# Performance work log

Measured on AMD Instinct MI355X. Metric: run time of the kernel, lower is better.

The kernel has to match this reference:

```python
import jax, jax.numpy as jnp
import numpy as np
from jax import lax

B, C_IN, N, C_OUT, K = 8, 64, 4096, 64, 20
EPS = 1e-5
NEG_SLOPE = 0.2


def setup_inputs() -> dict:
    key = jax.random.key(0)
    k1, k2, k3, k4, k5, k6 = jax.random.split(key, 6)
    x = jax.random.normal(k1, (B, C_IN, N), dtype=jnp.float32)
    # Conv2d(2*C_in, C_out, kernel_size=1, bias=False) -> weight (C_out, 2*C_in)
    W = jax.random.normal(k2, (C_OUT, 2 * C_IN), dtype=jnp.float32) * (1.0 / np.sqrt(2 * C_IN))
    gamma = jax.random.normal(k3, (C_OUT,), dtype=jnp.float32) * 0.1 + 1.0
    beta = jax.random.normal(k4, (C_OUT,), dtype=jnp.float32) * 0.1
    running_mean = jax.random.normal(k5, (C_OUT,), dtype=jnp.float32) * 0.1
    running_var = jax.random.uniform(k6, (C_OUT,), dtype=jnp.float32, minval=0.5, maxval=1.5)
    return {"x": x, "W": W, "gamma": gamma, "beta": beta,
            "running_mean": running_mean, "running_var": running_var}


def reference(x, W, gamma, beta, running_mean, running_var):
    # x: (B, C, N)
    # ---- KNN graph: pairwise squared distances, top-k nearest (includes self) ----
    xx = jnp.sum(x * x, axis=1)                       # (B, N)
    inner = jnp.einsum('bcn,bcm->bnm', x, x)          # (B, N, N)
    d2 = xx[:, :, None] - 2.0 * inner + xx[:, None, :]  # (B, N, N)
    _, idx = lax.top_k(-d2, K)                        # (B, N, K) int32 indices

    # ---- gather neighbor features ----
    xt = jnp.transpose(x, (0, 2, 1))                  # (B, N, C)
    neighbors = jax.vmap(lambda feats, i: feats[i])(xt, idx)  # (B, N, K, C)
    central = xt[:, :, None, :]                       # (B, N, 1, C) broadcast over K

    # ---- edge features: [x_i, x_j - x_i] -> (B, N, K, 2C) ----
    edge = jnp.concatenate(
        [jnp.broadcast_to(central, (B, N, K, C_IN)), neighbors - central], axis=-1)

    # ---- 1x1 conv (pointwise matmul) + BatchNorm (eval mode) + LeakyReLU ----
    h = jnp.einsum('bnkc,oc->bnko', edge, W)          # (B, N, K, C_out)
    inv_std = lax.rsqrt(running_var + EPS)
    h = (h - running_mean) * (inv_std * gamma) + beta
    h = jnp.where(h >= 0, h, NEG_SLOPE * h)           # LeakyReLU(0.2)

    # ---- max over k neighbors, return (B, C_out, N) ----
    out = jnp.max(h, axis=2)                          # (B, N, C_out)
    return jnp.transpose(out, (0, 2, 1))
```

## Files before the change

### kernel.cpp

```cpp
#include <hip/hip_runtime.h>

#define NB 8
#define NC 64
#define NN 4096
#define NO 64
#define KK 20
#define EPSV 1e-5f
#define SLOPE 0.2f

typedef __attribute__((ext_vector_type(8))) short short8x;
typedef __attribute__((ext_vector_type(4))) float float4x;


__device__ __forceinline__ unsigned short bfh(float f) {
  unsigned u = __float_as_uint(f);
  unsigned r = u + 0x7FFFu + ((u >> 16) & 1u);
  return (unsigned short)(r >> 16);
}

__device__ __forceinline__ unsigned flipf(float f) {
  unsigned u = __float_as_uint(f);
  return u ^ ((unsigned)((int)u >> 31) | 0x80000000u);
}

__device__ __forceinline__ unsigned unflipu(unsigned v) {
  return v ^ (0x80000000u | (unsigned)((int)(~v) >> 31));
}

__device__ __forceinline__ void gld_lds16(const unsigned short* g, unsigned short* l) {
  __builtin_amdgcn_global_load_lds(
      (const __attribute__((address_space(1))) unsigned int*)g,
      (__attribute__((address_space(3))) unsigned int*)l, 16, 0, 0);
}

__global__ void k0_wprep(const float* __restrict__ W,
                         float* __restrict__ wa, float* __restrict__ wb) {
  int t = threadIdx.x;
  for (int i = t; i < NC * NO; i += 256) {
    int o = i & 63, c = i >> 6;
    float w1 = W[o * 128 + c];
    float w2 = W[o * 128 + 64 + c];
    wa[i] = w1 - w2;
    wb[i] = w2;
  }
}

__global__ __launch_bounds__(256) void k1_feat(const float* __restrict__ x,
    const float* __restrict__ waT, const float* __restrict__ wbT,
    float* __restrict__ y1, float* __restrict__ y2, float* __restrict__ xxg,
    unsigned short* __restrict__ xThi, unsigned short* __restrict__ xTmid,
    unsigned short* __restrict__ xTlo) {
  __shared__ __align__(16) float xs[NC * 68];
  __shared__ __align__(16) float wa[NC * NO];
  __shared__ __align__(16) float wb[NC * NO];
  int t = threadIdx.x;
  int b = blockIdx.x >> 6;
  int gr0 = (blockIdx.x & 63) << 6;
  const float* xb = x + (size_t)b * NC * NN;
  #pragma unroll
  for (int k = 0; k < 4; ++k) {
    int i4 = t + k * 256;
    int c = i4 >> 4, col4 = (i4 & 15) << 2;
    *(float4*)&xs[c * 68 + col4] = *(const float4*)&xb[(size_t)c * NN + gr0 + col4];
    *(float4*)&wa[c * 64 + col4] = *(const float4*)&waT[c * 64 + col4];
    *(float4*)&wb[c * 64 + col4] = *(const float4*)&wbT[c * 64 + col4];
  }
  __syncthreads();
  if (t < 64) {
    float s = 0.f;
    #pragma unroll
    for (int c = 0; c < NC; ++c) { float v = xs[c * 68 + t]; s = fmaf(v, v, s); }
    xxg[b * NN + gr0 + t] = s;
  }
  int o = t & 63, w = t >> 6;
  for (int j = 0; j < 16; ++j) {
    int n = j * 4 + w;
    float a1 = 0.f, a2 = 0.f;
    #pragma unroll
    for (int c = 0; c < NC; ++c) {
      float xv = xs[c * 68 + n];
      a1 = fmaf(wa[c * 64 + o], xv, a1);
      a2 = fmaf(wb[c * 64 + o], xv, a2);
    }
    size_t base = ((size_t)b * NN + gr0 + n) * NO + o;
    y1[base] = a1;
    y2[base] = a2;
  }
  int n2 = t >> 2, c0 = (t & 3) << 4;
  short8x vh[2], vm[2], vl[2];
  #pragma unroll
  for (int i = 0; i < 16; ++i) {
    float v = xs[(c0 + i) * 68 + n2];
    unsigned short h = bfh(v);
    float hf = __uint_as_float((unsigned)h << 16);
    float r1 = v - hf;
    unsigned short md = bfh(r1);
    float mf = __uint_as_float((unsigned)md << 16);
    unsigned short lo = bfh(r1 - mf);
    vh[i >> 3][i & 7] = (short)h;
    vm[i >> 3][i & 7] = (short)md;
    vl[i >> 3][i & 7] = (short)lo;
  }
  size_t tb = ((size_t)(b * NN + gr0 + n2)) * 64 + c0;
  *(short8x*)&xThi[tb] = vh[0];  *(short8x*)&xThi[tb + 8] = vh[1];
  *(short8x*)&xTmid[tb] = vm[0]; *(short8x*)&xTmid[tb + 8] = vm[1];
  *(short8x*)&xTlo[tb] = vl[0];  *(short8x*)&xTlo[tb + 8] = vl[1];
}

__global__ __launch_bounds__(256, 3) void k2_topk(
    const unsigned short* __restrict__ xThi, const unsigned short* __restrict__ xTmid,
    const unsigned short* __restrict__ xTlo, const float* __restrict__ xxg,
    unsigned* __restrict__ keyuG, unsigned short* __restrict__ idxG) {
  __shared__ __align__(16) unsigned short Rb[3 * 4096];
  __shared__ __align__(16) float xxs[64];

  int t = threadIdx.x;
  int blk = blockIdx.x;
  int b = blk >> 7;
  int rem = blk & 127;
  int rg = rem >> 1, half = rem & 1;
  int gr0 = rg << 6;
  int gc0 = half << 11;
  int w = t >> 6;
  int l = t & 63;
  int lm = t & 15;
  int quad = (t >> 4) & 3;

  size_t abase = ((size_t)(b * NN + gr0 + 16 * w + lm)) * 64;
  short8x Ah[2], Am[2], Al[2];
  #pragma unroll
  for (int ks = 0; ks < 2; ++ks) {
    int co = ks * 32 + quad * 8;
    Ah[ks] = *(const short8x*)&xThi[abase + co];
    Am[ks] = *(const short8x*)&xTmid[abase + co];
    Al[ks] = *(const short8x*)&xTlo[abase + co];
  }

  unsigned long long lst[KK];
  #pragma unroll
  for (int j = 0; j < KK; ++j) lst[j] = ~0ull;

  size_t bbase = (size_t)(b * NN) * 64;
  int nof = ((l & 7) - (l >> 3)) & 7;
  int nrow = 16 * w + (l >> 3);
  unsigned short* ldst = &Rb[(2 * w) * 512];

  for (int mt = 0; mt < 32; ++mt) {
    int gm0 = gc0 + (mt << 6);
    __syncthreads();
    #pragma unroll
    for (int lvl = 0; lvl < 3; ++lvl) {
      const unsigned short* src = (lvl == 0) ? xThi : (lvl == 1) ? xTmid : xTlo;
      #pragma unroll
      for (int p = 0; p < 2; ++p) {
        gld_lds16(&src[bbase + (size_t)(gm0 + nrow + 8 * p) * 64 + nof * 8],
                  ldst + lvl * 4096 + p * 512);
      }
    }
    if (w == 0) {
      __builtin_amdgcn_global_load_lds(
          (const __attribute__((address_space(1))) unsigned int*)&xxg[b * NN + gm0 + l],
          (__attribute__((address_space(3))) unsigned int*)xxs, 4, 0, 0);
    }
    __syncthreads();

    float4x acc[4];
    #pragma unroll
    for (int j = 0; j < 4; ++j) acc[j] = (float4x){0.f, 0.f, 0.f, 0.f};

    const unsigned short* RbH = Rb;
    const unsigned short* RbM = Rb + 4096;
    const unsigned short* RbL = Rb + 8192;
    #pragma unroll
    for (int ks = 0; ks < 2; ++ks) {
      #pragma unroll
      for (int j = 0; j < 4; ++j) {
        int n = 16 * j + lm;
        int off = n * 64 + ((ks * 4 + quad + n) & 7) * 8;
        short8x bh = *(const short8x*)&RbH[off];
        short8x bm = *(const short8x*)&RbM[off];
        short8x bl = *(const short8x*)&RbL[off];
        acc[j] = __builtin_amdgcn_mfma_f32_16x16x32_bf16(bm, Am[ks], acc[j], 0, 0, 0);
        acc[j] = __builtin_amdgcn_mfma_f32_16x16x32_bf16(bl, Ah[ks], acc[j], 0, 0, 0);
        acc[j] = __builtin_amdgcn_mfma_f32_16x16x32_bf16(bh, Al[ks], acc[j], 0, 0, 0);
        acc[j] = __builtin_amdgcn_mfma_f32_16x16x32_bf16(bm, Ah[ks], acc[j], 0, 0, 0);
        acc[j] = __builtin_amdgcn_mfma_f32_16x16x32_bf16(bh, Am[ks], acc[j], 0, 0, 0);
        acc[j] = __builtin_amdgcn_mfma_f32_16x16x32_bf16(bh, Ah[ks], acc[j], 0, 0, 0);
      }
    }

    unsigned own19u = (unsigned)(lst[KK - 1] >> 12);
    own19u = min(own19u, 0xFF7FFFFFu);
    float thr = __uint_as_float(unflipu(own19u));
    thr = fminf(thr, __shfl_xor(thr, 16));
    thr = fminf(thr, __shfl_xor(thr, 32));

    unsigned mask = 0;
    #pragma unroll
    for (int j = 0; j < 4; ++j) {
      float4 xq = *(const float4*)&xxs[16 * j + 4 * quad];
      const float* xqp = (const float*)&xq;
      #pragma unroll
      for (int q = 0; q < 4; ++q) {
        float kv = fmaf(-2.f, acc[j][q], xqp[q]);
        mask |= (unsigned)(kv <= thr) << (4 * j + q);
      }
    }

    while (mask) {
      int e = __builtin_ctz(mask);
      mask &= mask - 1;
      float a00 = (e & 1) ? acc[0][1] : acc[0][0];
      float a01 = (e & 1) ? acc[0][3] : acc[0][2];
      float a10 = (e & 1) ? acc[1][1] : acc[1][0];
      float a11 = (e & 1) ? acc[1][3] : acc[1][2];
      float a20 = (e & 1) ? acc[2][1] : acc[2][0];
      float a21 = (e & 1) ? acc[2][3] : acc[2][2];
      float a30 = (e & 1) ? acc[3][1] : acc[3][0];
      float a31 = (e & 1) ? acc[3][3] : acc[3][2];
      float b0 = (e & 2) ? a01 : a00;
      float b1 = (e & 2) ? a11 : a10;
      float b2 = (e & 2) ? a21 : a20;
      float b3 = (e & 2) ? a31 : a30;
      float c0v = (e & 4) ? b1 : b0;
      float c1v = (e & 4) ? b3 : b2;
      float av = (e & 8) ? c1v : c0v;
      int c = ((e & 12) << 2) | (quad << 2) | (e & 3);
      float kv = fmaf(-2.f, av, xxs[c]);
      unsigned ku = flipf(kv);
      unsigned long long p = ((unsigned long long)ku << 12) | (unsigned)(gm0 + c);
      if (p < lst[KK - 1]) {
        #pragma unroll
        for (int jj = KK - 1; jj >= 1; --jj) {
          bool sh = p < lst[jj - 1];
          unsigned long long cur = (p < lst[jj]) ? p : lst[jj];
          lst[jj] = sh ? lst[jj - 1] : cur;
        }
        if (p < lst[0]) lst[0] = p;
      }
    }
  }

  int orow = 16 * w + lm, oq = quad;
  unsigned long long* M = (unsigned long long*)Rb;
  #pragma unroll 1
  for (int ph = 0; ph < 2; ++ph) {
    __syncthreads();
    if ((orow >> 5) == ph) {
      int r5 = orow & 31;
      #pragma unroll
      for (int k = 0; k < KK; ++k) M[r5 * 84 + oq * 21 + k] = lst[k];
      M[r5 * 84 + oq * 21 + KK] = ~0ull;
    }
    __syncthreads();
    if (t < 32) {
      int h0 = 0, h1 = 0, h2 = 0, h3 = 0;
      int rb = t * 84;
      int row = ph * 32 + t;
      size_t base = ((size_t)(b * NN + gr0 + row) * 2 + half) * KK;
      for (int k = 0; k < KK; ++k) {
        unsigned long long v0m = M[rb + h0];
        unsigned long long v1m = M[rb + 21 + h1];
        unsigned long long v2m = M[rb + 42 + h2];
        unsigned long long v3m = M[rb + 63 + h3];
        unsigned long long bv = v0m; int bq = 0;
        if (v1m < bv) { bv = v1m; bq = 1; }
        if (v2m < bv) { bv = v2m; bq = 2; }
        if (v3m < bv) { bv = v3m; bq = 3; }
        keyuG[base + k] = (unsigned)(bv >> 12);
        idxG[base + k] = (unsigned short)(bv & 0xFFFu);
        if (bq == 0) h0++; else if (bq == 1) h1++; else if (bq == 2) h2++; else h3++;
      }
    }
  }
}

__global__ __launch_bounds__(256) void k3_out(const float* __restrict__ y1,
    const float* __restrict__ y2, const unsigned* __restrict__ keyuG,
    const unsigned short* __restrict__ idxG,
    const float* __restrict__ gamma, const float* __restrict__ beta,
    const float* __restrict__ rmean, const float* __restrict__ rvar,
    float* __restrict__ out) {
  __shared__ int sidx[64 * KK];
  __shared__ float ot[64 * 65];
  int t = threadIdx.x;
  int b = blockIdx.x >> 6;
  int gr0 = (blockIdx.x & 63) << 6;
  if (t < 64) {
    size_t base0 = ((size_t)(b * NN + gr0 + t) * 2) * KK;
    size_t base1 = base0 + KK;
    int h0 = 0, h1 = 0;
    for (int k = 0; k < KK; ++k) {
      int a0 = h0 < KK ? h0 : KK - 1;
      int a1 = h1 < KK ? h1 : KK - 1;
      unsigned k0v = keyuG[base0 + a0]; unsigned i0 = idxG[base0 + a0];
      unsigned k1v = keyuG[base1 + a1]; unsigned i1 = idxG[base1 + a1];
      bool take0 = (h1 >= KK) ||
                   ((h0 < KK) && (k0v < k1v || (k0v == k1v && i0 < i1)));
      sidx[t * KK + k] = take0 ? (int)i0 : (int)i1;
      if (take0) h0++; else h1++;
    }
  }
  int l = t & 63, w = t >> 6;
  float sc = gamma[l] * rsqrtf(rvar[l] + EPSV);
  float tt = fmaf(-rmean[l], sc, beta[l]);
  __syncthreads();
  const float* y2b = y2 + (size_t)b * NN * NO;
  for (int rr = 0; rr < 16; ++rr) {
    int row = w * 16 + rr;
    float v1 = y1[((size_t)b * NN + gr0 + row) * NO + l];
    int mk[KK];
    #pragma unroll
    for (int k = 0; k < KK; ++k) mk[k] = sidx[row * KK + k];
    float vv[KK];
    #pragma unroll
    for (int k = 0; k < KK; ++k) vv[k] = y2b[(size_t)mk[k] * NO + l];
    float best = -3.4e38f;
    #pragma unroll
    for (int k = 0; k < KK; ++k) {
      float v = v1 + vv[k];
      v = fmaf(v, sc, tt);
      v = v >= 0.f ? v : SLOPE * v;
      best = fmaxf(best, v);
    }
    ot[l * 65 + row] = best;
  }
  __syncthreads();
  float* ob = out + (size_t)b * NO * NN;
  for (int i = t; i < 4096; i += 256) {
    int o = i >> 6, n = i & 63;
    ob[(size_t)o * NN + gr0 + n] = ot[o * 65 + n];
  }
}

extern "C" void kernel_launch(void* const* d_in, const int* in_sizes, int n_in,
                              void* d_out, int out_size, void* d_ws, size_t ws_size,
                              hipStream_t stream) {
  const float* x     = (const float*)d_in[0];
  const float* W     = (const float*)d_in[1];
  const float* gamma = (const float*)d_in[2];
  const float* beta  = (const float*)d_in[3];
  const float* rmean = (const float*)d_in[4];
  const float* rvar  = (const float*)d_in[5];
  float* ws  = (float*)d_ws;
  float* y1    = ws;
  float* y2    = ws + 2097152;
  float* xx    = ws + 4194304;
  unsigned* keyu = (unsigned*)(ws + 4227072);
  unsigned short* idxu = (unsigned short*)(ws + 5537792);
  float* wa    = ws + 6193152;
  float* wb    = ws + 6197248;
  unsigned short* xThi  = (unsigned short*)(ws + 6201344);
  unsigned short* xTmid = (unsigned short*)(ws + 7249920);
  unsigned short* xTlo  = (unsigned short*)(ws + 8298496);
  float* out = (float*)d_out;

  hipLaunchKernelGGL(k0_wprep, dim3(1),    dim3(256), 0, stream, W, wa, wb);
  hipLaunchKernelGGL(k1_feat,  dim3(512),  dim3(256), 0, stream, x, wa, wb, y1, y2, xx,
                     xThi, xTmid, xTlo);
  hipLaunchKernelGGL(k2_topk,  dim3(1024), dim3(256), 0, stream, xThi, xTmid, xTlo,
                     xx, keyu, idxu);
  hipLaunchKernelGGL(k3_out,   dim3(512),  dim3(256), 0, stream, y1, y2, keyu, idxu,
                     gamma, beta, rmean, rvar, out);
}
```

Baseline: 388.1 us.

## Double-buffer LDS tiles in top-k kernel to prefetch next column tile

Splits the shared-memory staging buffers for the hi/mid/lo bf16 column tiles and the squared-norm slice into two halves. A prologue loads the first tile. Each iteration then issues the async global-to-LDS loads for the next tile before running the MFMA distance computation and the top-k insertion on the current tile. This is meant to hide global load latency behind compute and the serial insertion loop. The cost is double the LDS footprint, which could limit occupancy, and the barrier still waits on the outstanding loads once per iteration.

```diff
diff --git a/kernel.cpp b/kernel.cpp
--- a/kernel.cpp
+++ b/kernel.cpp
@@ -111,8 +111,8 @@
     const unsigned short* __restrict__ xThi, const unsigned short* __restrict__ xTmid,
     const unsigned short* __restrict__ xTlo, const float* __restrict__ xxg,
     unsigned* __restrict__ keyuG, unsigned short* __restrict__ idxG) {
-  __shared__ __align__(16) unsigned short Rb[3 * 4096];
-  __shared__ __align__(16) float xxs[64];
+  __shared__ __align__(16) unsigned short Rb[2][3 * 4096];
+  __shared__ __align__(16) float xxs[2][64];
 
   int t = threadIdx.x;
   int blk = blockIdx.x;
@@ -143,34 +143,55 @@
   size_t bbase = (size_t)(b * NN) * 64;
   int nof = ((l & 7) - (l >> 3)) & 7;
   int nrow = 16 * w + (l >> 3);
-  unsigned short* ldst = &Rb[(2 * w) * 512];
-
-  for (int mt = 0; mt < 32; ++mt) {
-    int gm0 = gc0 + (mt << 6);
-    __syncthreads();
+
+  {
+    int gm0 = gc0;
     #pragma unroll
     for (int lvl = 0; lvl < 3; ++lvl) {
       const unsigned short* src = (lvl == 0) ? xThi : (lvl == 1) ? xTmid : xTlo;
       #pragma unroll
       for (int p = 0; p < 2; ++p) {
         gld_lds16(&src[bbase + (size_t)(gm0 + nrow + 8 * p) * 64 + nof * 8],
-                  ldst + lvl * 4096 + p * 512);
+                  &Rb[0][lvl * 4096 + (2 * w + p) * 512]);
       }
     }
     if (w == 0) {
       __builtin_amdgcn_global_load_lds(
           (const __attribute__((address_space(1))) unsigned int*)&xxg[b * NN + gm0 + l],
-          (__attribute__((address_space(3))) unsigned int*)xxs, 4, 0, 0);
-    }
+          (__attribute__((address_space(3))) unsigned int*)&xxs[0][0], 4, 0, 0);
+    }
+  }
+
+  for (int mt = 0; mt < 32; ++mt) {
+    int cur = mt & 1;
+    int gm0 = gc0 + (mt << 6);
     __syncthreads();
 
+    if (mt < 31) {
+      int gm1 = gm0 + 64;
+      #pragma unroll
+      for (int lvl = 0; lvl < 3; ++lvl) {
+        const unsigned short* src = (lvl == 0) ? xThi : (lvl == 1) ? xTmid : xTlo;
+        #pragma unroll
+        for (int p = 0; p < 2; ++p) {
+          gld_lds16(&src[bbase + (size_t)(gm1 + nrow + 8 * p) * 64 + nof * 8],
+                    &Rb[cur ^ 1][lvl * 4096 + (2 * w + p) * 512]);
+        }
+      }
+      if (w == 0) {
+        __builtin_amdgcn_global_load_lds(
+            (const __attribute__((address_space(1))) unsigned int*)&xxg[b * NN + gm1 + l],
+            (__attribute__((address_space(3))) unsigned int*)&xxs[cur ^ 1][0], 4, 0, 0);
+      }
+    }
+
     float4x acc[4];
     #pragma unroll
     for (int j = 0; j < 4; ++j) acc[j] = (float4x){0.f, 0.f, 0.f, 0.f};
 
-    const unsigned short* RbH = Rb;
-    const unsigned short* RbM = Rb + 4096;
-    const unsigned short* RbL = Rb + 8192;
+    const unsigned short* RbH = &Rb[cur][0];
+    const unsigned short* RbM = &Rb[cur][4096];
+    const unsigned short* RbL = &Rb[cur][8192];
     #pragma unroll
     for (int ks = 0; ks < 2; ++ks) {
       #pragma unroll
@@ -195,10 +216,11 @@
     thr = fminf(thr, __shfl_xor(thr, 16));
     thr = fminf(thr, __shfl_xor(thr, 32));
 
+    const float* xxc = &xxs[cur][0];
     unsigned mask = 0;
     #pragma unroll
     for (int j = 0; j < 4; ++j) {
-      float4 xq = *(const float4*)&xxs[16 * j + 4 * quad];
+      float4 xq = *(const float4*)&xxc[16 * j + 4 * quad];
       const float* xqp = (const float*)&xq;
       #pragma unroll
       for (int q = 0; q < 4; ++q) {
@@ -226,15 +248,15 @@
       float c1v = (e & 4) ? b3 : b2;
       float av = (e & 8) ? c1v : c0v;
       int c = ((e & 12) << 2) | (quad << 2) | (e & 3);
-      float kv = fmaf(-2.f, av, xxs[c]);
+      float kv = fmaf(-2.f, av, xxc[c]);
       unsigned ku = flipf(kv);
       unsigned long long p = ((unsigned long long)ku << 12) | (unsigned)(gm0 + c);
       if (p < lst[KK - 1]) {
         #pragma unroll
         for (int jj = KK - 1; jj >= 1; --jj) {
           bool sh = p < lst[jj - 1];
-          unsigned long long cur = (p < lst[jj]) ? p : lst[jj];
-          lst[jj] = sh ? lst[jj - 1] : cur;
+          unsigned long long curv = (p < lst[jj]) ? p : lst[jj];
+          lst[jj] = sh ? lst[jj - 1] : curv;
         }
         if (p < lst[0]) lst[0] = p;
       }
@@ -242,7 +264,7 @@
   }
 
   int orow = 16 * w + lm, oq = quad;
-  unsigned long long* M = (unsigned long long*)Rb;
+  unsigned long long* M = (unsigned long long*)&Rb[0][0];
   #pragma unroll 1
   for (int ph = 0; ph < 2; ++ph) {
     __syncthreads();
```

Result: no change. 389.8 us (+0.4%).
